# Optimization experiments

Measured on AMD Instinct MI355X. Metric: run time of the kernel, lower is better.

Reference implementation:

```python
import jax, jax.numpy as jnp
import numpy as np

H = 2048      # hidden_size
I = 8192      # intermediate_size
NH = 16       # num_heads
HD = H // NH  # head_dim
EPS = 1e-6


def setup_inputs() -> dict:
    key = jax.random.key(0)
    ks = jax.random.split(key, 10)
    s = 0.02
    return {
        "hidden_states": jax.random.normal(ks[0], (2, 2048, H), dtype=jnp.float32),
        "wq": jax.random.normal(ks[1], (H, H), dtype=jnp.float32) * s,
        "wk": jax.random.normal(ks[2], (H, H), dtype=jnp.float32) * s,
        "wv": jax.random.normal(ks[3], (H, H), dtype=jnp.float32) * s,
        "wo": jax.random.normal(ks[4], (H, H), dtype=jnp.float32) * s,
        "w_gate": jax.random.normal(ks[5], (H, I), dtype=jnp.float32) * s,
        "w_up": jax.random.normal(ks[6], (H, I), dtype=jnp.float32) * s,
        "w_down": jax.random.normal(ks[7], (I, H), dtype=jnp.float32) * s,
        "ln1_w": jnp.ones((H,), dtype=jnp.float32),
        "ln2_w": jnp.ones((H,), dtype=jnp.float32),
    }


def rmsnorm(x, w):
    xf = x.astype(jnp.float32)
    var = jnp.mean(xf * xf, axis=-1, keepdims=True)
    return w * (xf * jax.lax.rsqrt(var + EPS)).astype(x.dtype)


def reference(hidden_states, wq, wk, wv, wo, w_gate, w_up, w_down, ln1_w, ln2_w):
    b, s, _ = hidden_states.shape
    residual = hidden_states
    x = rmsnorm(hidden_states, ln1_w)

    # attention (no RoPE, no causal mask, per source)
    q = (x @ wq).reshape(b, s, NH, HD)
    k = (x @ wk).reshape(b, s, NH, HD)
    v = (x @ wv).reshape(b, s, NH, HD)
    scores = jnp.einsum('bqhd,bkhd->bhqk', q, k) / jnp.sqrt(jnp.float32(HD))
    attn = jax.nn.softmax(scores, axis=-1)
    out = jnp.einsum('bhqk,bkhd->bqhd', attn, v).reshape(b, s, H)
    hidden = residual + out @ wo

    residual = hidden
    y = rmsnorm(hidden, ln2_w)
    gate = jax.nn.silu(y @ w_gate)
    up = y @ w_up
    return residual + (gate * up) @ w_down
```

## Files before the change

### kernel.cpp

```cpp
#include <hip/hip_runtime.h>
#include <hip/hip_bf16.h>

#define HDIM 2048
#define IDIM 8192
#define NHEADS 16
#define HEADD 128
#define BATCH 2
#define SEQ 2048
#define MTOK 4096

typedef unsigned short u16;
typedef __bf16 bf16x8 __attribute__((ext_vector_type(8)));
typedef float f32x4 __attribute__((ext_vector_type(4)));
typedef float f32x16 __attribute__((ext_vector_type(16)));
typedef unsigned short u16x8 __attribute__((ext_vector_type(8)));
typedef unsigned int u32x2 __attribute__((ext_vector_type(2)));
typedef unsigned int u32x4 __attribute__((ext_vector_type(4)));
typedef unsigned int uv2 __attribute__((ext_vector_type(2)));

__device__ __forceinline__ u16 f2b(float f) {
  unsigned u = __builtin_bit_cast(unsigned, f);
  u += 0x7FFFu + ((u >> 16) & 1u);
  return (u16)(u >> 16);
}
__device__ __forceinline__ float b2f(u16 b) {
  unsigned u = ((unsigned)b) << 16;
  return __builtin_bit_cast(float, u);
}
__device__ __forceinline__ void gl_lds16(const void* g, void* l) {
  auto gp = (const __attribute__((address_space(1))) unsigned int*)((unsigned long long)g);
  auto lp = (__attribute__((address_space(3))) unsigned int*)((unsigned)(unsigned long long)l);
  __builtin_amdgcn_global_load_lds(gp, lp, 16, 0, 0);
}
__device__ __forceinline__ unsigned cvtpk(float lo, float hi) {
  unsigned r;
  asm("v_cvt_pk_bf16_f32 %0, %1, %2" : "=v"(r) : "v"(lo), "v"(hi));
  return r;
}

__global__ __launch_bounds__(256) void wtrans_all(const float* __restrict__ wq, const float* __restrict__ wk,
                                                  const float* __restrict__ wv, const float* __restrict__ wo,
                                                  const float* __restrict__ wg, const float* __restrict__ wu,
                                                  const float* __restrict__ wd,
                                                  u16* __restrict__ wqkvT, u16* __restrict__ woT,
                                                  u16* __restrict__ wgT, u16* __restrict__ wuT,
                                                  u16* __restrict__ wdT) {
  int bidf = blockIdx.x;
  const float* W;
  u16* Wt;
  int K, N, rowoff, bx, by;
  if (bidf < 3072) {
    int s = bidf >> 10, r = bidf & 1023;
    W = s == 0 ? wq : (s == 1 ? wk : wv);
    Wt = wqkvT; K = 2048; N = 2048; rowoff = s * 2048;
    bx = r & 31; by = r >> 5;
  } else if (bidf < 4096) {
    int r = bidf - 3072;
    W = wo; Wt = woT; K = 2048; N = 2048; rowoff = 0;
    bx = r & 31; by = r >> 5;
  } else if (bidf < 8192) {
    int r = bidf - 4096;
    W = wg; Wt = wgT; K = 2048; N = 8192; rowoff = 0;
    bx = r & 127; by = r >> 7;
  } else if (bidf < 12288) {
    int r = bidf - 8192;
    W = wu; Wt = wuT; K = 2048; N = 8192; rowoff = 0;
    bx = r & 127; by = r >> 7;
  } else {
    int r = bidf - 12288;
    W = wd; Wt = wdT; K = 8192; N = 2048; rowoff = 0;
    bx = r & 31; by = r >> 5;
  }
  __shared__ float t[64][65];
  int n0 = bx * 64, k0 = by * 64;
  int tid = threadIdx.x;
  int kr = tid >> 4, nc = (tid & 15) * 4;
#pragma unroll
  for (int p = 0; p < 4; p++) {
    float4 v = *(const float4*)&W[(size_t)(k0 + p * 16 + kr) * N + n0 + nc];
    t[nc + 0][p * 16 + kr] = v.x;
    t[nc + 1][p * 16 + kr] = v.y;
    t[nc + 2][p * 16 + kr] = v.z;
    t[nc + 3][p * 16 + kr] = v.w;
  }
  __syncthreads();
  int n = tid >> 2, kq = (tid & 3) * 16;
  u16 tmp[16];
#pragma unroll
  for (int i = 0; i < 16; i++) tmp[i] = f2b(t[n][kq + i]);
  *(u16x8*)&Wt[(size_t)(rowoff + n0 + n) * K + k0 + kq] = *(u16x8*)&tmp[0];
  *(u16x8*)&Wt[(size_t)(rowoff + n0 + n) * K + k0 + kq + 8] = *(u16x8*)&tmp[8];
}

__global__ __launch_bounds__(256) void vtrans_k(const u16* __restrict__ qkv, u16* __restrict__ vt) {
  __shared__ u16 t[32][33];
  int s0 = blockIdx.x * 32, d0 = blockIdx.y * 32, bh = blockIdx.z;
  int b = bh >> 4, h = bh & 15;
  int tx = threadIdx.x, ty = threadIdx.y;
#pragma unroll
  for (int i = 0; i < 4; i++)
    t[ty + i * 8][tx] = qkv[(size_t)(b * SEQ + s0 + ty + i * 8) * 6144 + 4096 + h * HEADD + d0 + tx];
  __syncthreads();
#pragma unroll
  for (int i = 0; i < 4; i++)
    vt[(size_t)(bh * HEADD + d0 + ty + i * 8) * SEQ + s0 + tx] = t[tx][ty + i * 8];
}

__global__ __launch_bounds__(256) void rmsnorm_k(const float* __restrict__ X, const float* __restrict__ W,
                                                 u16* __restrict__ O) {
  int row = blockIdx.x;
  int tid = threadIdx.x;
  const float* x = X + (size_t)row * HDIM;
  float4 v0 = ((const float4*)x)[tid * 2];
  float4 v1 = ((const float4*)x)[tid * 2 + 1];
  float ss = v0.x * v0.x + v0.y * v0.y + v0.z * v0.z + v0.w * v0.w
           + v1.x * v1.x + v1.y * v1.y + v1.z * v1.z + v1.w * v1.w;
#pragma unroll
  for (int off = 32; off > 0; off >>= 1) ss += __shfl_down(ss, off);
  __shared__ float red[4];
  if ((tid & 63) == 0) red[tid >> 6] = ss;
  __syncthreads();
  float rs = rsqrtf((red[0] + red[1] + red[2] + red[3]) * (1.0f / HDIM) + 1e-6f);
  const float* w = W + tid * 8;
  u16* o = O + (size_t)row * HDIM + tid * 8;
  float vals[8] = {v0.x, v0.y, v0.z, v0.w, v1.x, v1.y, v1.z, v1.w};
#pragma unroll
  for (int j = 0; j < 8; j++) o[j] = f2b(w[j] * vals[j] * rs);
}

template <int EPI>
__global__ __launch_bounds__(512, 2) void gemm_s(const u16* __restrict__ A, const u16* __restrict__ Bt,
                                                 int M, int N, int K,
                                                 u16* __restrict__ Cb, float* __restrict__ Cf,
                                                 const float* __restrict__ Res) {
  __shared__ char lds[98304];
  const int tid = threadIdx.x, lane = tid & 63, w = tid >> 6;
  const int wm = w >> 2, wn = w & 3;
  const int GX = gridDim.x;
  const int bid = blockIdx.y * GX + blockIdx.x;
  const int xcd = bid & 7, ii = bid >> 3;
  const int j = ii & 31, rin = ii >> 5;
  const int rectIdx = rin * 8 + xcd;
  const int nry = gridDim.y >> 2;
  const int ry = rectIdx % nry, rx = rectIdx / nry;
  const int by = ry * 4 + (j >> 3), bx = rx * 8 + (j & 7);
  const int m0 = by * 256, n0 = bx * 128;
  const int NT = K >> 6;

  const int srow = w * 8 + (lane >> 3);
  const int kko = ((lane & 7) ^ (lane >> 3)) * 8;
  const u16* Asrc = A + (size_t)(m0 + srow) * K + kko;
  const u16* Bsrc = Bt + (size_t)(n0 + srow) * K + kko;
  const int wofs = w * 1024;

#define SSA(buf, kt)                                                                  \
  {                                                                                   \
    gl_lds16(Asrc + (size_t)(kt) * 64, lds + (buf) * 49152 + wofs);                   \
    gl_lds16(Asrc + 64 * (size_t)K + (size_t)(kt) * 64, lds + (buf) * 49152 + 8192 + wofs);   \
    gl_lds16(Asrc + 128 * (size_t)K + (size_t)(kt) * 64, lds + (buf) * 49152 + 16384 + wofs); \
    gl_lds16(Asrc + 192 * (size_t)K + (size_t)(kt) * 64, lds + (buf) * 49152 + 24576 + wofs); \
  }
#define SSB(buf, kt)                                                                  \
  {                                                                                   \
    gl_lds16(Bsrc + (size_t)(kt) * 64, lds + (buf) * 49152 + 32768 + wofs);           \
    gl_lds16(Bsrc + 64 * (size_t)K + (size_t)(kt) * 64, lds + (buf) * 49152 + 40960 + wofs);  \
  }

  const int l15 = lane & 15, l4 = lane >> 4;
  const int kq0 = ((l4) ^ (l15 & 7)) << 4;
  const int kq1 = ((4 + l4) ^ (l15 & 7)) << 4;
  const int abase = wm * 16384 + l15 * 128;
  const int bbase = 32768 + (wn * 32 + l15) * 128;

  const f32x4 fz = {0.f, 0.f, 0.f, 0.f};
  f32x4 acc[8][2];
#pragma unroll
  for (int i = 0; i < 8; i++) { acc[i][0] = fz; acc[i][1] = fz; }
  bf16x8 af[8], bq0[2], bq1[2];

  SSA(0, 0);
  SSB(0, 0);
  asm volatile("s_waitcnt vmcnt(2)" ::: "memory");
  __builtin_amdgcn_s_barrier();

  for (int t = 0; t < NT; ++t) {
    const int buf = t & 1, nb = buf ^ 1;
    const char* Lb = lds + buf * 49152;
    const int t1 = (t + 1 < NT) ? t + 1 : NT - 1;
#pragma unroll
    for (int mf = 0; mf < 8; mf++) af[mf] = *(const bf16x8*)(Lb + abase + mf * 2048 + kq0);
    SSA(nb, t1);
    asm volatile("s_waitcnt vmcnt(4)" ::: "memory");
    __builtin_amdgcn_s_barrier();
    bq0[0] = *(const bf16x8*)(Lb + bbase + kq0);
    bq0[1] = *(const bf16x8*)(Lb + bbase + 2048 + kq0);
    bq1[0] = *(const bf16x8*)(Lb + bbase + kq1);
    bq1[1] = *(const bf16x8*)(Lb + bbase + 2048 + kq1);
    asm volatile("s_waitcnt lgkmcnt(0)" ::: "memory");
    __builtin_amdgcn_sched_barrier(0);
    __builtin_amdgcn_s_setprio(1);
#pragma unroll
    for (int mf = 0; mf < 8; mf++) {
      acc[mf][0] = __builtin_amdgcn_mfma_f32_16x16x32_bf16(af[mf], bq0[0], acc[mf][0], 0, 0, 0);
      acc[mf][1] = __builtin_amdgcn_mfma_f32_16x16x32_bf16(af[mf], bq0[1], acc[mf][1], 0, 0, 0);
    }
    __builtin_amdgcn_s_setprio(0);
#pragma unroll
    for (int mf = 0; mf < 8; mf++) af[mf] = *(const bf16x8*)(Lb + abase + mf * 2048 + kq1);
    SSB(nb, t1);
    asm volatile("s_waitcnt vmcnt(2)" ::: "memory");
    asm volatile("s_waitcnt lgkmcnt(0)" ::: "memory");
    __builtin_amdgcn_sched_barrier(0);
    __builtin_amdgcn_s_barrier();
    __builtin_amdgcn_s_setprio(1);
#pragma unroll
    for (int mf = 0; mf < 8; mf++) {
      acc[mf][0] = __builtin_amdgcn_mfma_f32_16x16x32_bf16(af[mf], bq1[0], acc[mf][0], 0, 0, 0);
      acc[mf][1] = __builtin_amdgcn_mfma_f32_16x16x32_bf16(af[mf], bq1[1], acc[mf][1], 0, 0, 0);
    }
    __builtin_amdgcn_s_setprio(0);
  }
  asm volatile("s_waitcnt vmcnt(0)" ::: "memory");

#pragma unroll
  for (int mf = 0; mf < 8; mf++) {
#pragma unroll
    for (int jr = 0; jr < 4; jr++) {
      const int m = m0 + wm * 128 + mf * 16 + l4 * 4 + jr;
#pragma unroll
      for (int nf = 0; nf < 2; nf++) {
        const int n = n0 + wn * 32 + nf * 16 + l15;
        float v = acc[mf][nf][jr];
        size_t idx = (size_t)m * N + n;
        if (EPI == 0) {
          Cb[idx] = f2b(v);
        } else {
          Cf[idx] = Res[idx] + v;
        }
      }
    }
  }
#undef SSA
#undef SSB
}

__global__ __launch_bounds__(512, 2) void gemm_fgu(const u16* __restrict__ A, const u16* __restrict__ Bg,
                                                   const u16* __restrict__ Bu, u16* __restrict__ G) {
  __shared__ char lds[131072];
  const int tid = threadIdx.x, lane = tid & 63, w = tid >> 6;
  const int wm = w >> 2, wn = w & 3;
  const int bid = blockIdx.y * 64 + blockIdx.x;
  const int xcd = bid & 7, ii = bid >> 3;
  const int j = ii & 31, rin = ii >> 5;
  const int rectIdx = rin * 8 + xcd;
  const int ry = rectIdx & 3, rx = rectIdx >> 2;
  const int by = ry * 4 + (j >> 3), bx = rx * 8 + (j & 7);
  const int m0 = by * 256, n0 = bx * 128;
  const int NT = 32;

  const int srow = w * 8 + (lane >> 3);
  const int kko = ((lane & 7) ^ (lane >> 3)) * 8;
  const u16* Asrc = A + (size_t)(m0 + srow) * 2048 + kko;
  const u16* Bgsrc = Bg + (size_t)(n0 + srow) * 2048 + kko;
  const u16* Busrc = Bu + (size_t)(n0 + srow) * 2048 + kko;
  const int wofs = w * 1024;

#define SA0(buf, kt)                                                        \
  {                                                                         \
    gl_lds16(Asrc + (kt) * 64, lds + (buf) * 65536 + wofs);                 \
    gl_lds16(Asrc + 64 * 2048 + (kt) * 64, lds + (buf) * 65536 + 8192 + wofs); \
  }
#define SA1(buf, kt)                                                              \
  {                                                                               \
    gl_lds16(Asrc + 128 * 2048 + (kt) * 64, lds + (buf) * 65536 + 16384 + wofs);  \
    gl_lds16(Asrc + 192 * 2048 + (kt) * 64, lds + (buf) * 65536 + 24576 + wofs);  \
  }
#define SBG(buf, kt)                                                              \
  {                                                                               \
    gl_lds16(Bgsrc + (kt) * 64, lds + (buf) * 65536 + 32768 + wofs);              \
    gl_lds16(Bgsrc + 64 * 2048 + (kt) * 64, lds + (buf) * 65536 + 40960 + wofs);  \
  }
#define SBU(buf, kt)                                                              \
  {                                                                               \
    gl_lds16(Busrc + (kt) * 64, lds + (buf) * 65536 + 49152 + wofs);              \
    gl_lds16(Busrc + 64 * 2048 + (kt) * 64, lds + (buf) * 65536 + 57344 + wofs);  \
  }
#define LG0 { asm volatile("s_waitcnt lgkmcnt(0)" ::: "memory"); __builtin_amdgcn_sched_barrier(0); }

  const int l15 = lane & 15, l4 = lane >> 4;
  const int kq0 = ((l4) ^ (l15 & 7)) << 4;
  const int kq1 = ((4 + l4) ^ (l15 & 7)) << 4;
  const int abase = (wm * 128 + l15) * 128;
  const int gbase = 32768 + (wn * 32 + l15) * 128;
  const int ubase = 49152 + (wn * 32 + l15) * 128;

  const f32x4 fz = {0.f, 0.f, 0.f, 0.f};
  f32x4 ag[8][2], au[8][2];
#pragma unroll
  for (int i = 0; i < 8; i++)
#pragma unroll
    for (int jj = 0; jj < 2; jj++) { ag[i][jj] = fz; au[i][jj] = fz; }
  bf16x8 af[8], bgf[2], buf2[2];

  SA0(0, 0);
  SBG(0, 0);
  SA1(0, 0);
  SBU(0, 0);
  asm volatile("s_waitcnt vmcnt(2)" ::: "memory");
  __builtin_amdgcn_s_barrier();

  for (int t = 0; t < NT; ++t) {
    const int buf = t & 1, nb = buf ^ 1;
    const char* Lb = lds + buf * 65536;
    const int t1 = (t + 1 < NT) ? t + 1 : NT - 1;
#pragma unroll
    for (int mf = 0; mf < 8; mf++) af[mf] = *(const bf16x8*)(Lb + abase + mf * 2048 + kq0);
    bgf[0] = *(const bf16x8*)(Lb + gbase + kq0);
    bgf[1] = *(const bf16x8*)(Lb + gbase + 2048 + kq0);
    SA0(nb, t1);
    SBG(nb, t1);
    __builtin_amdgcn_s_barrier();
    LG0;
    __builtin_amdgcn_s_setprio(1);
#pragma unroll
    for (int mf = 0; mf < 8; mf++) {
      ag[mf][0] = __builtin_amdgcn_mfma_f32_16x16x32_bf16(af[mf], bgf[0], ag[mf][0], 0, 0, 0);
      ag[mf][1] = __builtin_amdgcn_mfma_f32_16x16x32_bf16(af[mf], bgf[1], ag[mf][1], 0, 0, 0);
    }
    __builtin_amdgcn_s_setprio(0);
    asm volatile("s_waitcnt vmcnt(4)" ::: "memory");
    __builtin_amdgcn_s_barrier();
    buf2[0] = *(const bf16x8*)(Lb + ubase + kq0);
    buf2[1] = *(const bf16x8*)(Lb + ubase + 2048 + kq0);
    SA1(nb, t1);
    __builtin_amdgcn_s_barrier();
    LG0;
    __builtin_amdgcn_s_setprio(1);
#pragma unroll
    for (int mf = 0; mf < 8; mf++) {
      au[mf][0] = __builtin_amdgcn_mfma_f32_16x16x32_bf16(af[mf], buf2[0], au[mf][0], 0, 0, 0);
      au[mf][1] = __builtin_amdgcn_mfma_f32_16x16x32_bf16(af[mf], buf2[1], au[mf][1], 0, 0, 0);
    }
    __builtin_amdgcn_s_setprio(0);
    __builtin_amdgcn_s_barrier();
#pragma unroll
    for (int mf = 0; mf < 8; mf++) af[mf] = *(const bf16x8*)(Lb + abase + mf * 2048 + kq1);
    bgf[0] = *(const bf16x8*)(Lb + gbase + kq1);
    bgf[1] = *(const bf16x8*)(Lb + gbase + 2048 + kq1);
    __builtin_amdgcn_s_barrier();
    LG0;
    __builtin_amdgcn_s_setprio(1);
#pragma unroll
    for (int mf = 0; mf < 8; mf++) {
      ag[mf][0] = __builtin_amdgcn_mfma_f32_16x16x32_bf16(af[mf], bgf[0], ag[mf][0], 0, 0, 0);
      ag[mf][1] = __builtin_amdgcn_mfma_f32_16x16x32_bf16(af[mf], bgf[1], ag[mf][1], 0, 0, 0);
    }
    __builtin_amdgcn_s_setprio(0);
    __builtin_amdgcn_s_barrier();
    buf2[0] = *(const bf16x8*)(Lb + ubase + kq1);
    buf2[1] = *(const bf16x8*)(Lb + ubase + 2048 + kq1);
    SBU(nb, t1);
    __builtin_amdgcn_s_barrier();
    LG0;
    __builtin_amdgcn_s_setprio(1);
#pragma unroll
    for (int mf = 0; mf < 8; mf++) {
      au[mf][0] = __builtin_amdgcn_mfma_f32_16x16x32_bf16(af[mf], buf2[0], au[mf][0], 0, 0, 0);
      au[mf][1] = __builtin_amdgcn_mfma_f32_16x16x32_bf16(af[mf], buf2[1], au[mf][1], 0, 0, 0);
    }
    __builtin_amdgcn_s_setprio(0);
    asm volatile("s_waitcnt vmcnt(2)" ::: "memory");
    __builtin_amdgcn_s_barrier();
  }
  asm volatile("s_waitcnt vmcnt(0)" ::: "memory");

#pragma unroll
  for (int mf = 0; mf < 8; mf++) {
#pragma unroll
    for (int jr = 0; jr < 4; jr++) {
      const int m = m0 + wm * 128 + mf * 16 + l4 * 4 + jr;
#pragma unroll
      for (int nf = 0; nf < 2; nf++) {
        const int n = n0 + wn * 32 + nf * 16 + l15;
        float g = ag[mf][nf][jr];
        float u = au[mf][nf][jr];
        float sg = g / (1.f + __expf(-g));
        G[(size_t)m * IDIM + n] = f2b(sg * u);
      }
    }
  }
#undef SA0
#undef SA1
#undef SBG
#undef SBU
#undef LG0
}

__global__ __launch_bounds__(512, 2) void attn_k(const u16* __restrict__ qkv, const u16* __restrict__ vt,
                                                 u16* __restrict__ out) {
  __shared__ char Kl[2][16384];
  __shared__ char Vl[2][16384];
  int tid = threadIdx.x, lane = tid & 63, w = tid >> 6;
  int bid = blockIdx.y * 8 + blockIdx.x;
  int swz = (bid & 7) * 32 + (bid >> 3);
  int qb = swz & 7, bh = swz >> 3;
  int b = bh >> 4, h = bh & 15;
  int l31 = lane & 31, hi = lane >> 5;
  const float c = 0.088388347648318447f * 1.4426950408889634f;
  const float RT = 90.51f;

  const int qrow = qb * 256 + w * 32 + l31;
  bf16x8 q[8];
  {
    const u16* qp = qkv + (size_t)(b * SEQ + qrow) * 6144 + h * HEADD + hi * 8;
#pragma unroll
    for (int dt = 0; dt < 8; dt++) q[dt] = *(const bf16x8*)(qp + dt * 16);
  }
  f32x16 o[4];
#pragma unroll
  for (int i = 0; i < 4; i++)
#pragma unroll
    for (int j = 0; j < 16; j++) o[i][j] = 0.f;
  float mrow = -1e30f, lrow = 0.f;

#define ASTAGE(buf, t)                                                                     \
  {                                                                                        \
    int kv0_ = (t) * 64;                                                                   \
    _Pragma("unroll") for (int i = 0; i < 2; i++) {                                        \
      int r = w * 8 + i * 4 + (lane >> 4);                                                 \
      int col = ((lane & 15) ^ (r & 15)) * 8;                                              \
      const u16* src = qkv + (size_t)(b * SEQ + kv0_ + r) * 6144 + HDIM + h * HEADD + col; \
      gl_lds16(src, &Kl[buf][(w * 8 + i * 4) * 256]);                                      \
    }                                                                                      \
    _Pragma("unroll") for (int i = 0; i < 2; i++) {                                        \
      int d = w * 16 + i * 8 + (lane >> 3);                                                \
      int col = ((lane & 7) ^ (d & 7)) * 8;                                                \
      const u16* src = vt + (size_t)(bh * HEADD + d) * SEQ + kv0_ + col;                   \
      gl_lds16(src, &Vl[buf][(w * 16 + i * 8) * 128]);                                     \
    }                                                                                      \
  }

  ASTAGE(0, 0);
  __syncthreads();

  for (int t = 0; t < SEQ / 64; t++) {
    const int buf = t & 1;
    if (t + 1 < SEQ / 64) ASTAGE(buf ^ 1, t + 1);
    const char* Kb = &Kl[buf][0];
    const char* Vb = &Vl[buf][0];
    f32x16 s0, s1;
#pragma unroll
    for (int j = 0; j < 16; j++) { s0[j] = 0.f; s1[j] = 0.f; }
    const int ksl = l31 & 15;
    __builtin_amdgcn_s_setprio(1);
#pragma unroll
    for (int dt = 0; dt < 8; dt++) {
      bf16x8 k0 = *(const bf16x8*)(Kb + (l31)*256 + (((dt * 2 + hi) ^ ksl) << 4));
      bf16x8 k1 = *(const bf16x8*)(Kb + (32 + l31) * 256 + (((dt * 2 + hi) ^ ksl) << 4));
      s0 = __builtin_amdgcn_mfma_f32_32x32x16_bf16(k0, q[dt], s0, 0, 0, 0);
      s1 = __builtin_amdgcn_mfma_f32_32x32x16_bf16(k1, q[dt], s1, 0, 0, 0);
    }
    __builtin_amdgcn_s_setprio(0);
    float m8[8];
#pragma unroll
    for (int g = 0; g < 4; g++) {
      m8[g] = fmaxf(fmaxf(s0[4 * g], s0[4 * g + 1]), fmaxf(s0[4 * g + 2], s0[4 * g + 3]));
      m8[4 + g] = fmaxf(fmaxf(s1[4 * g], s1[4 * g + 1]), fmaxf(s1[4 * g + 2], s1[4 * g + 3]));
    }
    float vmax = fmaxf(fmaxf(fmaxf(m8[0], m8[1]), fmaxf(m8[2], m8[3])),
                       fmaxf(fmaxf(m8[4], m8[5]), fmaxf(m8[6], m8[7])));
    {
      uv2 pr = __builtin_amdgcn_permlane32_swap(__builtin_bit_cast(unsigned, vmax),
                                                __builtin_bit_cast(unsigned, vmax), false, false);
      vmax = fmaxf(__builtin_bit_cast(float, pr[0]), __builtin_bit_cast(float, pr[1]));
    }
    if (__any(vmax > mrow + RT)) {
      float mnew = fmaxf(mrow, vmax);
      float alpha = exp2f((mrow - mnew) * c);
      mrow = mnew;
      lrow *= alpha;
#pragma unroll
      for (int i = 0; i < 4; i++)
#pragma unroll
        for (int j = 0; j < 16; j++) o[i][j] *= alpha;
    }
    const float mc = mrow * c;
    float r4[4] = {0.f, 0.f, 0.f, 0.f};
#pragma unroll
    for (int j = 0; j < 16; j++) {
      s0[j] = exp2f(s0[j] * c - mc);
      r4[j & 3] += s0[j];
    }
#pragma unroll
    for (int j = 0; j < 16; j++) {
      s1[j] = exp2f(s1[j] * c - mc);
      r4[j & 3] += s1[j];
    }
    float rsum = (r4[0] + r4[1]) + (r4[2] + r4[3]);
    {
      uv2 pr = __builtin_amdgcn_permlane32_swap(__builtin_bit_cast(unsigned, rsum),
                                                __builtin_bit_cast(unsigned, rsum), false, false);
      rsum = __builtin_bit_cast(float, pr[0]) + __builtin_bit_cast(float, pr[1]);
    }
    lrow += rsum;
    bf16x8 pa[4];
#pragma unroll
    for (int half = 0; half < 2; half++) {
      const f32x16& sv = half ? s1 : s0;
#pragma unroll
      for (int blk = 0; blk < 2; blk++) {
        int base = blk * 8;
        unsigned A = cvtpk(sv[base + 0], sv[base + 1]);
        unsigned B = cvtpk(sv[base + 2], sv[base + 3]);
        unsigned C = cvtpk(sv[base + 4], sv[base + 5]);
        unsigned D = cvtpk(sv[base + 6], sv[base + 7]);
        uv2 ac = __builtin_amdgcn_permlane32_swap(A, C, false, false);
        uv2 bd = __builtin_amdgcn_permlane32_swap(B, D, false, false);
        u32x4 w4;
        w4[0] = ac[0]; w4[1] = bd[0]; w4[2] = ac[1]; w4[3] = bd[1];
        pa[half * 2 + blk] = __builtin_bit_cast(bf16x8, w4);
      }
    }
    __builtin_amdgcn_s_setprio(1);
#pragma unroll
    for (int dt4 = 0; dt4 < 4; dt4++) {
      const char* vbase = Vb + (dt4 * 32 + l31) * 128;
      const int vsl = l31 & 7;
#pragma unroll
      for (int ks = 0; ks < 4; ks++) {
        bf16x8 vb = *(const bf16x8*)(vbase + (((ks * 2 + hi) ^ vsl) << 4));
        o[dt4] = __builtin_amdgcn_mfma_f32_32x32x16_bf16(vb, pa[ks], o[dt4], 0, 0, 0);
      }
    }
    __builtin_amdgcn_s_setprio(0);
    __syncthreads();
  }
#undef ASTAGE

  const float linv = 1.0f / lrow;
  u16* orow = out + (size_t)(b * SEQ + qrow) * HDIM + h * HEADD;
#pragma unroll
  for (int dt4 = 0; dt4 < 4; dt4++) {
#pragma unroll
    for (int g = 0; g < 4; g++) {
      u32x2 st;
      st[0] = cvtpk(o[dt4][4 * g + 0] * linv, o[dt4][4 * g + 1] * linv);
      st[1] = cvtpk(o[dt4][4 * g + 2] * linv, o[dt4][4 * g + 3] * linv);
      *(u32x2*)(orow + dt4 * 32 + 8 * g + 4 * hi) = st;
    }
  }
}

extern "C" void kernel_launch(void* const* d_in, const int* in_sizes, int n_in,
                              void* d_out, int out_size, void* d_ws, size_t ws_size,
                              hipStream_t stream) {
  const float* hs  = (const float*)d_in[0];
  const float* wq  = (const float*)d_in[1];
  const float* wk  = (const float*)d_in[2];
  const float* wv  = (const float*)d_in[3];
  const float* wo  = (const float*)d_in[4];
  const float* wg  = (const float*)d_in[5];
  const float* wu  = (const float*)d_in[6];
  const float* wd  = (const float*)d_in[7];
  const float* ln1 = (const float*)d_in[8];
  const float* ln2 = (const float*)d_in[9];
  char* ws = (char*)d_ws;
  u16*   wqkvT = (u16*)(ws);
  u16*   woT   = (u16*)(ws + 25165824ull);
  u16*   wgT   = (u16*)(ws + 33554432ull);
  u16*   wuT   = (u16*)(ws + 67108864ull);
  u16*   wdT   = (u16*)(ws + 100663296ull);
  u16*   xb    = (u16*)(ws + 134217728ull);
  float* hid   = (float*)(ws + 150994944ull);
  u16*   qkv   = (u16*)(ws + 184549376ull);
  u16*   vtb   = (u16*)(ws + 234881024ull);
  u16*   attn  = (u16*)(ws + 251658368ull);
  u16*   g     = qkv;

  wtrans_all<<<16384, 256, 0, stream>>>(wq, wk, wv, wo, wg, wu, wd, wqkvT, woT, wgT, wuT, wdT);

  rmsnorm_k<<<MTOK, 256, 0, stream>>>(hs, ln1, xb);
  gemm_s<0><<<dim3(48, 16), 512, 0, stream>>>(xb, wqkvT, MTOK, 6144, HDIM, qkv, nullptr, nullptr);
  vtrans_k<<<dim3(64, 4, 32), dim3(32, 8), 0, stream>>>(qkv, vtb);
  attn_k<<<dim3(8, 32), 512, 0, stream>>>(qkv, vtb, attn);
  gemm_s<3><<<dim3(16, 16), 512, 0, stream>>>(attn, woT, MTOK, HDIM, HDIM, nullptr, hid, hs);
  rmsnorm_k<<<MTOK, 256, 0, stream>>>(hid, ln2, xb);
  gemm_fgu<<<dim3(64, 16), 512, 0, stream>>>(xb, wgT, wuT, g);
  gemm_s<3><<<dim3(16, 16), 512, 0, stream>>>(g, wdT, MTOK, HDIM, IDIM, nullptr, (float*)d_out, hid);
}
```

Before: 723.7 us.

## Use 64x64 wave tiles in GEMMs and merge gate/up K-steps in fused MLP

The generic GEMM changes its wave layout from 2x4 (128x32 per wave) to 4x2 (64x64 per wave). Each wave now reads 4 A and 4 B fragments per k-slice instead of 8 A and 2 B, which cuts LDS read traffic per MFMA. The gate/up fused GEMM is rewritten so that each half k-step loads the A tile and both gate and up B fragments together. It then issues gate and up MFMAs back to back, going from four barrier-separated phases per tile to two. The rewrite needs more fragment registers, which could hurt occupancy at the 2-blocks launch bound.

```diff
diff --git a/kernel.cpp b/kernel.cpp
--- a/kernel.cpp
+++ b/kernel.cpp
@@ -36,6 +36,16 @@
   unsigned r;
   asm("v_cvt_pk_bf16_f32 %0, %1, %2" : "=v"(r) : "v"(lo), "v"(hi));
   return r;
+}
+__device__ __forceinline__ void rect_swz(int gx, int gy, int& bx, int& by) {
+  const int bid = blockIdx.y * gx + blockIdx.x;
+  const int xcd = bid & 7, ii = bid >> 3;
+  const int j = ii & 31, rin = ii >> 5;
+  const int rectIdx = rin * 8 + xcd;
+  const int nry = gy >> 2;
+  const int ry = rectIdx % nry, rx = rectIdx / nry;
+  by = ry * 4 + (j >> 3);
+  bx = rx * 8 + (j & 7);
 }
 
 __global__ __launch_bounds__(256) void wtrans_all(const float* __restrict__ wq, const float* __restrict__ wk,
@@ -129,21 +139,15 @@
 }
 
 template <int EPI>
-__global__ __launch_bounds__(512, 2) void gemm_s(const u16* __restrict__ A, const u16* __restrict__ Bt,
-                                                 int M, int N, int K,
-                                                 u16* __restrict__ Cb, float* __restrict__ Cf,
-                                                 const float* __restrict__ Res) {
+__global__ __launch_bounds__(512, 2) void gemm_lean(const u16* __restrict__ A, const u16* __restrict__ Bt,
+                                                    int M, int N, int K,
+                                                    u16* __restrict__ Cb, float* __restrict__ Cf,
+                                                    const float* __restrict__ Res) {
   __shared__ char lds[98304];
   const int tid = threadIdx.x, lane = tid & 63, w = tid >> 6;
-  const int wm = w >> 2, wn = w & 3;
-  const int GX = gridDim.x;
-  const int bid = blockIdx.y * GX + blockIdx.x;
-  const int xcd = bid & 7, ii = bid >> 3;
-  const int j = ii & 31, rin = ii >> 5;
-  const int rectIdx = rin * 8 + xcd;
-  const int nry = gridDim.y >> 2;
-  const int ry = rectIdx % nry, rx = rectIdx / nry;
-  const int by = ry * 4 + (j >> 3), bx = rx * 8 + (j & 7);
+  const int wm = w >> 1, wn = w & 1;
+  int bx, by;
+  rect_swz(gridDim.x, gridDim.y, bx, by);
   const int m0 = by * 256, n0 = bx * 128;
   const int NT = K >> 6;
 
@@ -153,30 +157,33 @@
   const u16* Bsrc = Bt + (size_t)(n0 + srow) * K + kko;
   const int wofs = w * 1024;
 
-#define SSA(buf, kt)                                                                  \
-  {                                                                                   \
-    gl_lds16(Asrc + (size_t)(kt) * 64, lds + (buf) * 49152 + wofs);                   \
+#define SSA(buf, kt)                                                                          \
+  {                                                                                           \
+    gl_lds16(Asrc + (size_t)(kt) * 64, lds + (buf) * 49152 + wofs);                           \
     gl_lds16(Asrc + 64 * (size_t)K + (size_t)(kt) * 64, lds + (buf) * 49152 + 8192 + wofs);   \
     gl_lds16(Asrc + 128 * (size_t)K + (size_t)(kt) * 64, lds + (buf) * 49152 + 16384 + wofs); \
     gl_lds16(Asrc + 192 * (size_t)K + (size_t)(kt) * 64, lds + (buf) * 49152 + 24576 + wofs); \
   }
-#define SSB(buf, kt)                                                                  \
-  {                                                                                   \
-    gl_lds16(Bsrc + (size_t)(kt) * 64, lds + (buf) * 49152 + 32768 + wofs);           \
-    gl_lds16(Bsrc + 64 * (size_t)K + (size_t)(kt) * 64, lds + (buf) * 49152 + 40960 + wofs);  \
-  }
+#define SSB(buf, kt)                                                                         \
+  {                                                                                          \
+    gl_lds16(Bsrc + (size_t)(kt) * 64, lds + (buf) * 49152 + 32768 + wofs);                  \
+    gl_lds16(Bsrc + 64 * (size_t)K + (size_t)(kt) * 64, lds + (buf) * 49152 + 40960 + wofs); \
+  }
+#define LG0 { asm volatile("s_waitcnt lgkmcnt(0)" ::: "memory"); __builtin_amdgcn_sched_barrier(0); }
 
   const int l15 = lane & 15, l4 = lane >> 4;
   const int kq0 = ((l4) ^ (l15 & 7)) << 4;
   const int kq1 = ((4 + l4) ^ (l15 & 7)) << 4;
-  const int abase = wm * 16384 + l15 * 128;
-  const int bbase = 32768 + (wn * 32 + l15) * 128;
+  const int abase = (wm * 64 + l15) * 128;
+  const int bbase = 32768 + (wn * 64 + l15) * 128;
 
   const f32x4 fz = {0.f, 0.f, 0.f, 0.f};
-  f32x4 acc[8][2];
-#pragma unroll
-  for (int i = 0; i < 8; i++) { acc[i][0] = fz; acc[i][1] = fz; }
-  bf16x8 af[8], bq0[2], bq1[2];
+  f32x4 acc[4][4];
+#pragma unroll
+  for (int i = 0; i < 4; i++)
+#pragma unroll
+    for (int jj = 0; jj < 4; jj++) acc[i][jj] = fz;
+  bf16x8 af0[4], af1[4], b0[4], b1[4];
 
   SSA(0, 0);
   SSB(0, 0);
@@ -188,48 +195,46 @@
     const char* Lb = lds + buf * 49152;
     const int t1 = (t + 1 < NT) ? t + 1 : NT - 1;
 #pragma unroll
-    for (int mf = 0; mf < 8; mf++) af[mf] = *(const bf16x8*)(Lb + abase + mf * 2048 + kq0);
+    for (int mf = 0; mf < 4; mf++) af0[mf] = *(const bf16x8*)(Lb + abase + mf * 2048 + kq0);
     SSA(nb, t1);
     asm volatile("s_waitcnt vmcnt(4)" ::: "memory");
     __builtin_amdgcn_s_barrier();
-    bq0[0] = *(const bf16x8*)(Lb + bbase + kq0);
-    bq0[1] = *(const bf16x8*)(Lb + bbase + 2048 + kq0);
-    bq1[0] = *(const bf16x8*)(Lb + bbase + kq1);
-    bq1[1] = *(const bf16x8*)(Lb + bbase + 2048 + kq1);
-    asm volatile("s_waitcnt lgkmcnt(0)" ::: "memory");
-    __builtin_amdgcn_sched_barrier(0);
+#pragma unroll
+    for (int nf = 0; nf < 4; nf++) b0[nf] = *(const bf16x8*)(Lb + bbase + nf * 2048 + kq0);
+    LG0;
     __builtin_amdgcn_s_setprio(1);
 #pragma unroll
-    for (int mf = 0; mf < 8; mf++) {
-      acc[mf][0] = __builtin_amdgcn_mfma_f32_16x16x32_bf16(af[mf], bq0[0], acc[mf][0], 0, 0, 0);
-      acc[mf][1] = __builtin_amdgcn_mfma_f32_16x16x32_bf16(af[mf], bq0[1], acc[mf][1], 0, 0, 0);
-    }
+    for (int mf = 0; mf < 4; mf++)
+#pragma unroll
+      for (int nf = 0; nf < 4; nf++)
+        acc[mf][nf] = __builtin_amdgcn_mfma_f32_16x16x32_bf16(af0[mf], b0[nf], acc[mf][nf], 0, 0, 0);
     __builtin_amdgcn_s_setprio(0);
 #pragma unroll
-    for (int mf = 0; mf < 8; mf++) af[mf] = *(const bf16x8*)(Lb + abase + mf * 2048 + kq1);
+    for (int mf = 0; mf < 4; mf++) af1[mf] = *(const bf16x8*)(Lb + abase + mf * 2048 + kq1);
+#pragma unroll
+    for (int nf = 0; nf < 4; nf++) b1[nf] = *(const bf16x8*)(Lb + bbase + nf * 2048 + kq1);
     SSB(nb, t1);
     asm volatile("s_waitcnt vmcnt(2)" ::: "memory");
-    asm volatile("s_waitcnt lgkmcnt(0)" ::: "memory");
-    __builtin_amdgcn_sched_barrier(0);
+    LG0;
     __builtin_amdgcn_s_barrier();
     __builtin_amdgcn_s_setprio(1);
 #pragma unroll
-    for (int mf = 0; mf < 8; mf++) {
-      acc[mf][0] = __builtin_amdgcn_mfma_f32_16x16x32_bf16(af[mf], bq1[0], acc[mf][0], 0, 0, 0);
-      acc[mf][1] = __builtin_amdgcn_mfma_f32_16x16x32_bf16(af[mf], bq1[1], acc[mf][1], 0, 0, 0);
-    }
+    for (int mf = 0; mf < 4; mf++)
+#pragma unroll
+      for (int nf = 0; nf < 4; nf++)
+        acc[mf][nf] = __builtin_amdgcn_mfma_f32_16x16x32_bf16(af1[mf], b1[nf], acc[mf][nf], 0, 0, 0);
     __builtin_amdgcn_s_setprio(0);
   }
   asm volatile("s_waitcnt vmcnt(0)" ::: "memory");
 
 #pragma unroll
-  for (int mf = 0; mf < 8; mf++) {
+  for (int mf = 0; mf < 4; mf++) {
 #pragma unroll
     for (int jr = 0; jr < 4; jr++) {
-      const int m = m0 + wm * 128 + mf * 16 + l4 * 4 + jr;
-#pragma unroll
-      for (int nf = 0; nf < 2; nf++) {
-        const int n = n0 + wn * 32 + nf * 16 + l15;
+      const int m = m0 + wm * 64 + mf * 16 + l4 * 4 + jr;
+#pragma unroll
+      for (int nf = 0; nf < 4; nf++) {
+        const int n = n0 + wn * 64 + nf * 16 + l15;
         float v = acc[mf][nf][jr];
         size_t idx = (size_t)m * N + n;
         if (EPI == 0) {
@@ -242,19 +247,16 @@
   }
 #undef SSA
 #undef SSB
-}
-
-__global__ __launch_bounds__(512, 2) void gemm_fgu(const u16* __restrict__ A, const u16* __restrict__ Bg,
-                                                   const u16* __restrict__ Bu, u16* __restrict__ G) {
+#undef LG0
+}
+
+__global__ __launch_bounds__(512, 2) void gemm_fgu2(const u16* __restrict__ A, const u16* __restrict__ Bg,
+                                                    const u16* __restrict__ Bu, u16* __restrict__ G) {
   __shared__ char lds[131072];
   const int tid = threadIdx.x, lane = tid & 63, w = tid >> 6;
   const int wm = w >> 2, wn = w & 3;
-  const int bid = blockIdx.y * 64 + blockIdx.x;
-  const int xcd = bid & 7, ii = bid >> 3;
-  const int j = ii & 31, rin = ii >> 5;
-  const int rectIdx = rin * 8 + xcd;
-  const int ry = rectIdx & 3, rx = rectIdx >> 2;
-  const int by = ry * 4 + (j >> 3), bx = rx * 8 + (j & 7);
+  int bx, by;
+  rect_swz(64, 16, bx, by);
   const int m0 = by * 256, n0 = bx * 128;
   const int NT = 32;
 
@@ -265,23 +267,17 @@
   const u16* Busrc = Bu + (size_t)(n0 + srow) * 2048 + kko;
   const int wofs = w * 1024;
 
-#define SA0(buf, kt)                                                        \
-  {                                                                         \
-    gl_lds16(Asrc + (kt) * 64, lds + (buf) * 65536 + wofs);                 \
-    gl_lds16(Asrc + 64 * 2048 + (kt) * 64, lds + (buf) * 65536 + 8192 + wofs); \
-  }
-#define SA1(buf, kt)                                                              \
+#define SSA(buf, kt)                                                              \
   {                                                                               \
+    gl_lds16(Asrc + (kt) * 64, lds + (buf) * 65536 + wofs);                       \
+    gl_lds16(Asrc + 64 * 2048 + (kt) * 64, lds + (buf) * 65536 + 8192 + wofs);    \
     gl_lds16(Asrc + 128 * 2048 + (kt) * 64, lds + (buf) * 65536 + 16384 + wofs);  \
     gl_lds16(Asrc + 192 * 2048 + (kt) * 64, lds + (buf) * 65536 + 24576 + wofs);  \
   }
-#define SBG(buf, kt)                                                              \
+#define SBGU(buf, kt)                                                             \
   {                                                                               \
     gl_lds16(Bgsrc + (kt) * 64, lds + (buf) * 65536 + 32768 + wofs);              \
     gl_lds16(Bgsrc + 64 * 2048 + (kt) * 64, lds + (buf) * 65536 + 40960 + wofs);  \
-  }
-#define SBU(buf, kt)                                                              \
-  {                                                                               \
     gl_lds16(Busrc + (kt) * 64, lds + (buf) * 65536 + 49152 + wofs);              \
     gl_lds16(Busrc + 64 * 2048 + (kt) * 64, lds + (buf) * 65536 + 57344 + wofs);  \
   }
@@ -300,13 +296,11 @@
   for (int i = 0; i < 8; i++)
 #pragma unroll
     for (int jj = 0; jj < 2; jj++) { ag[i][jj] = fz; au[i][jj] = fz; }
-  bf16x8 af[8], bgf[2], buf2[2];
-
-  SA0(0, 0);
-  SBG(0, 0);
-  SA1(0, 0);
-  SBU(0, 0);
-  asm volatile("s_waitcnt vmcnt(2)" ::: "memory");
+  bf16x8 af0[8], af1[8], bg0[2], bg1[2], bu0[2], bu1[2];
+
+  SSA(0, 0);
+  SBGU(0, 0);
+  asm volatile("s_waitcnt vmcnt(4)" ::: "memory");
   __builtin_amdgcn_s_barrier();
 
   for (int t = 0; t < NT; ++t) {
@@ -314,63 +308,43 @@
     const char* Lb = lds + buf * 65536;
     const int t1 = (t + 1 < NT) ? t + 1 : NT - 1;
 #pragma unroll
-    for (int mf = 0; mf < 8; mf++) af[mf] = *(const bf16x8*)(Lb + abase + mf * 2048 + kq0);
-    bgf[0] = *(const bf16x8*)(Lb + gbase + kq0);
-    bgf[1] = *(const bf16x8*)(Lb + gbase + 2048 + kq0);
-    SA0(nb, t1);
-    SBG(nb, t1);
+    for (int mf = 0; mf < 8; mf++) af0[mf] = *(const bf16x8*)(Lb + abase + mf * 2048 + kq0);
+    SSA(nb, t1);
+    asm volatile("s_waitcnt vmcnt(4)" ::: "memory");
     __builtin_amdgcn_s_barrier();
+    bg0[0] = *(const bf16x8*)(Lb + gbase + kq0);
+    bg0[1] = *(const bf16x8*)(Lb + gbase + 2048 + kq0);
+    bu0[0] = *(const bf16x8*)(Lb + ubase + kq0);
+    bu0[1] = *(const bf16x8*)(Lb + ubase + 2048 + kq0);
+    bg1[0] = *(const bf16x8*)(Lb + gbase + kq1);
+    bg1[1] = *(const bf16x8*)(Lb + gbase + 2048 + kq1);
+    bu1[0] = *(const bf16x8*)(Lb + ubase + kq1);
+    bu1[1] = *(const bf16x8*)(Lb + ubase + 2048 + kq1);
     LG0;
     __builtin_amdgcn_s_setprio(1);
 #pragma unroll
     for (int mf = 0; mf < 8; mf++) {
-      ag[mf][0] = __builtin_amdgcn_mfma_f32_16x16x32_bf16(af[mf], bgf[0], ag[mf][0], 0, 0, 0);
-      ag[mf][1] = __builtin_amdgcn_mfma_f32_16x16x32_bf16(af[mf], bgf[1], ag[mf][1], 0, 0, 0);
+      ag[mf][0] = __builtin_amdgcn_mfma_f32_16x16x32_bf16(af0[mf], bg0[0], ag[mf][0], 0, 0, 0);
+      ag[mf][1] = __builtin_amdgcn_mfma_f32_16x16x32_bf16(af0[mf], bg0[1], ag[mf][1], 0, 0, 0);
+      au[mf][0] = __builtin_amdgcn_mfma_f32_16x16x32_bf16(af0[mf], bu0[0], au[mf][0], 0, 0, 0);
+      au[mf][1] = __builtin_amdgcn_mfma_f32_16x16x32_bf16(af0[mf], bu0[1], au[mf][1], 0, 0, 0);
     }
     __builtin_amdgcn_s_setprio(0);
+#pragma unroll
+    for (int mf = 0; mf < 8; mf++) af1[mf] = *(const bf16x8*)(Lb + abase + mf * 2048 + kq1);
+    SBGU(nb, t1);
     asm volatile("s_waitcnt vmcnt(4)" ::: "memory");
+    LG0;
     __builtin_amdgcn_s_barrier();
-    buf2[0] = *(const bf16x8*)(Lb + ubase + kq0);
-    buf2[1] = *(const bf16x8*)(Lb + ubase + 2048 + kq0);
-    SA1(nb, t1);
-    __builtin_amdgcn_s_barrier();
-    LG0;
     __builtin_amdgcn_s_setprio(1);
 #pragma unroll
     for (int mf = 0; mf < 8; mf++) {
-      au[mf][0] = __builtin_amdgcn_mfma_f32_16x16x32_bf16(af[mf], buf2[0], au[mf][0], 0, 0, 0);
-      au[mf][1] = __builtin_amdgcn_mfma_f32_16x16x32_bf16(af[mf], buf2[1], au[mf][1], 0, 0, 0);
+      ag[mf][0] = __builtin_amdgcn_mfma_f32_16x16x32_bf16(af1[mf], bg1[0], ag[mf][0], 0, 0, 0);
+      ag[mf][1] = __builtin_amdgcn_mfma_f32_16x16x32_bf16(af1[mf], bg1[1], ag[mf][1], 0, 0, 0);
+      au[mf][0] = __builtin_amdgcn_mfma_f32_16x16x32_bf16(af1[mf], bu1[0], au[mf][0], 0, 0, 0);
+      au[mf][1] = __builtin_amdgcn_mfma_f32_16x16x32_bf16(af1[mf], bu1[1], au[mf][1], 0, 0, 0);
     }
     __builtin_amdgcn_s_setprio(0);
-    __builtin_amdgcn_s_barrier();
-#pragma unroll
-    for (int mf = 0; mf < 8; mf++) af[mf] = *(const bf16x8*)(Lb + abase + mf * 2048 + kq1);
-    bgf[0] = *(const bf16x8*)(Lb + gbase + kq1);
-    bgf[1] = *(const bf16x8*)(Lb + gbase + 2048 + kq1);
-    __builtin_amdgcn_s_barrier();
-    LG0;
-    __builtin_amdgcn_s_setprio(1);
-#pragma unroll
-    for (int mf = 0; mf < 8; mf++) {
-      ag[mf][0] = __builtin_amdgcn_mfma_f32_16x16x32_bf16(af[mf], bgf[0], ag[mf][0], 0, 0, 0);
-      ag[mf][1] = __builtin_amdgcn_mfma_f32_16x16x32_bf16(af[mf], bgf[1], ag[mf][1], 0, 0, 0);
-    }
-    __builtin_amdgcn_s_setprio(0);
-    __builtin_amdgcn_s_barrier();
-    buf2[0] = *(const bf16x8*)(Lb + ubase + kq1);
-    buf2[1] = *(const bf16x8*)(Lb + ubase + 2048 + kq1);
-    SBU(nb, t1);
-    __builtin_amdgcn_s_barrier();
-    LG0;
-    __builtin_amdgcn_s_setprio(1);
-#pragma unroll
-    for (int mf = 0; mf < 8; mf++) {
-      au[mf][0] = __builtin_amdgcn_mfma_f32_16x16x32_bf16(af[mf], buf2[0], au[mf][0], 0, 0, 0);
-      au[mf][1] = __builtin_amdgcn_mfma_f32_16x16x32_bf16(af[mf], buf2[1], au[mf][1], 0, 0, 0);
-    }
-    __builtin_amdgcn_s_setprio(0);
-    asm volatile("s_waitcnt vmcnt(2)" ::: "memory");
-    __builtin_amdgcn_s_barrier();
   }
   asm volatile("s_waitcnt vmcnt(0)" ::: "memory");
 
@@ -389,10 +363,8 @@
       }
     }
   }
-#undef SA0
-#undef SA1
-#undef SBG
-#undef SBU
+#undef SSA
+#undef SBGU
 #undef LG0
 }
 
@@ -580,11 +552,11 @@
   wtrans_all<<<16384, 256, 0, stream>>>(wq, wk, wv, wo, wg, wu, wd, wqkvT, woT, wgT, wuT, wdT);
 
   rmsnorm_k<<<MTOK, 256, 0, stream>>>(hs, ln1, xb);
-  gemm_s<0><<<dim3(48, 16), 512, 0, stream>>>(xb, wqkvT, MTOK, 6144, HDIM, qkv, nullptr, nullptr);
+  gemm_lean<0><<<dim3(48, 16), 512, 0, stream>>>(xb, wqkvT, MTOK, 6144, HDIM, qkv, nullptr, nullptr);
   vtrans_k<<<dim3(64, 4, 32), dim3(32, 8), 0, stream>>>(qkv, vtb);
   attn_k<<<dim3(8, 32), 512, 0, stream>>>(qkv, vtb, attn);
-  gemm_s<3><<<dim3(16, 16), 512, 0, stream>>>(attn, woT, MTOK, HDIM, HDIM, nullptr, hid, hs);
+  gemm_lean<3><<<dim3(16, 16), 512, 0, stream>>>(attn, woT, MTOK, HDIM, HDIM, nullptr, hid, hs);
   rmsnorm_k<<<MTOK, 256, 0, stream>>>(hid, ln2, xb);
-  gemm_fgu<<<dim3(64, 16), 512, 0, stream>>>(xb, wgT, wuT, g);
-  gemm_s<3><<<dim3(16, 16), 512, 0, stream>>>(g, wdT, MTOK, HDIM, IDIM, nullptr, (float*)d_out, hid);
-}
+  gemm_fgu2<<<dim3(64, 16), 512, 0, stream>>>(xb, wgT, wuT, g);
+  gemm_lean<3><<<dim3(16, 16), 512, 0, stream>>>(g, wdT, MTOK, HDIM, IDIM, nullptr, (float*)d_out, hid);
+}
```

Result: no change. 716.3 us (-1.0%).
